# Optimization experiments

Hardware: AMD Instinct MI355X
Metric: run time of the kernel (lower is better)

Reference implementation:

```python
import jax, jax.numpy as jnp
import numpy as np

H = 256
W = 256
P = 512

# spherical-harmonics constants (degree 0..3), as in the 3DGS CUDA kernel
C0 = 0.28209479177387814
C1 = 0.4886025119029199
C2 = [1.0925484305920792, -1.0925484305920792, 0.31539156525252005, -1.0925484305920792, 0.5462742152960396]
C3 = [-0.5900435899266435, 2.890611442640554, -0.4570457994644658, 0.3731763325901154, -0.4570457994644658, 1.445305721320277, -0.5900435899266435]


def _quat_to_rot(q):
    # q: [P,4] (w,x,y,z), normalized here as the kernel assumes unit quats
    q = q / jnp.linalg.norm(q, axis=-1, keepdims=True)
    w, x, y, z = q[:, 0], q[:, 1], q[:, 2], q[:, 3]
    R = jnp.stack([
        1 - 2 * (y * y + z * z), 2 * (x * y - w * z), 2 * (x * z + w * y),
        2 * (x * y + w * z), 1 - 2 * (x * x + z * z), 2 * (y * z - w * x),
        2 * (x * z - w * y), 2 * (y * z + w * x), 1 - 2 * (x * x + y * y)], axis=-1)
    return R.reshape(-1, 3, 3)


def _eval_sh(sh, d):
    # sh: [P,16,3], d: [P,3] unit view dirs -> RGB [P,3]
    x, y, z = d[:, 0:1], d[:, 1:2], d[:, 2:3]
    xx, yy, zz = x * x, y * y, z * z
    xy, yz, xz = x * y, y * z, x * z
    res = C0 * sh[:, 0]
    res = res - C1 * y * sh[:, 1] + C1 * z * sh[:, 2] - C1 * x * sh[:, 3]
    res = (res + C2[0] * xy * sh[:, 4] + C2[1] * yz * sh[:, 5]
           + C2[2] * (2 * zz - xx - yy) * sh[:, 6] + C2[3] * xz * sh[:, 7]
           + C2[4] * (xx - yy) * sh[:, 8])
    res = (res + C3[0] * y * (3 * xx - yy) * sh[:, 9] + C3[1] * xy * z * sh[:, 10]
           + C3[2] * y * (4 * zz - xx - yy) * sh[:, 11]
           + C3[3] * z * (2 * zz - 3 * xx - 3 * yy) * sh[:, 12]
           + C3[4] * x * (4 * zz - xx - yy) * sh[:, 13]
           + C3[5] * z * (xx - yy) * sh[:, 14] + C3[6] * x * (xx - 3 * yy) * sh[:, 15])
    return jnp.maximum(res + 0.5, 0.0)


def render(means_3d, features, opacities, scales, rotations, viewmatrix, projmatrix, campos, tanfovx, tanfovy):
    Rv = viewmatrix[:3, :3]
    tv = viewmatrix[:3, 3]
    t = means_3d @ Rv.T + tv            # camera-space positions [P,3]
    depth = t[:, 2]
    # 3D covariance = (R S)(R S)^T
    Rq = _quat_to_rot(rotations)
    M = Rq * scales[:, None, :]
    cov3 = M @ jnp.swapaxes(M, 1, 2)    # [P,3,3]
    # EWA 2D covariance via perspective Jacobian
    fx = W / (2.0 * tanfovx)
    fy = H / (2.0 * tanfovy)
    limx = 1.3 * tanfovx
    limy = 1.3 * tanfovy
    tz = depth
    txz = jnp.clip(t[:, 0] / tz, -limx, limx) * tz
    tyz = jnp.clip(t[:, 1] / tz, -limy, limy) * tz
    zeros = jnp.zeros_like(tz)
    J = jnp.stack([
        jnp.stack([fx / tz, zeros, -fx * txz / (tz * tz)], -1),
        jnp.stack([zeros, fy / tz, -fy * tyz / (tz * tz)], -1)], 1)  # [P,2,3]
    T = J @ Rv
    cov2 = T @ cov3 @ jnp.swapaxes(T, 1, 2)  # [P,2,2]
    a = cov2[:, 0, 0] + 0.3  # low-pass dilation as in 3DGS
    b = cov2[:, 0, 1]
    c = cov2[:, 1, 1] + 0.3
    det = a * c - b * b
    inv_det = 1.0 / jnp.where(det > 0, det, 1.0)
    conic_a = c * inv_det
    conic_b = -b * inv_det
    conic_c = a * inv_det
    # project means to pixel coords
    ph = jnp.concatenate([means_3d, jnp.ones_like(depth)[:, None]], 1)
    pp = ph @ projmatrix.T
    pw = pp[:, 3] + 1e-7
    px = ((pp[:, 0] / pw + 1.0) * W - 1.0) * 0.5
    py = ((pp[:, 1] / pw + 1.0) * H - 1.0) * 0.5
    # SH -> RGB with view direction
    dirs = means_3d - campos
    dirs = dirs / jnp.linalg.norm(dirs, axis=-1, keepdims=True)
    colors = _eval_sh(features, dirs)   # [P,3]
    valid = (depth > 0.2) & (det > 0)
    # global front-to-back depth sort (kernel does per-tile; one global tile here)
    order = jnp.argsort(depth)
    px, py = px[order], py[order]
    conic_a, conic_b, conic_c = conic_a[order], conic_b[order], conic_c[order]
    colors = colors[order]
    opa = opacities[:, 0][order]
    valid = valid[order]
    # per-pixel alpha compositing
    ys, xs = jnp.meshgrid(jnp.arange(H, dtype=px.dtype), jnp.arange(W, dtype=px.dtype), indexing='ij')
    pix_x = xs.reshape(-1)              # [HW]
    pix_y = ys.reshape(-1)
    dx = pix_x[:, None] - px[None, :]   # [HW,P]
    dy = pix_y[:, None] - py[None, :]
    power = -0.5 * (conic_a[None, :] * dx * dx + conic_c[None, :] * dy * dy) - conic_b[None, :] * dx * dy
    alpha = jnp.minimum(0.99, opa[None, :] * jnp.exp(power))
    alpha = jnp.where((power <= 0.0) & valid[None, :] & (alpha >= 1.0 / 255.0), alpha, 0.0)
    Tcum = jnp.cumprod(1.0 - alpha, axis=1)                 # transmittance after gaussian i
    T_excl = jnp.concatenate([jnp.ones((alpha.shape[0], 1), alpha.dtype), Tcum[:, :-1]], 1)
    wgt = alpha * T_excl                                    # [HW,P]
    bg = jnp.ones((3,), dtype=alpha.dtype)                  # bg_color = (1,1,1) as in module
    out = wgt @ colors + Tcum[:, -1:] * bg[None, :]         # [HW,3]
    return out.T.reshape(3, H, W)


def setup_inputs() -> dict:
    key = jax.random.key(0)
    k = jax.random.split(key, 5)
    means_3d = jax.random.normal(k[0], (P, 3), jnp.float32) * jnp.array([1.5, 1.5, 0.8]) + jnp.array([0.0, 0.0, 5.0])
    features = jax.random.normal(k[1], (P, 16, 3), jnp.float32) * 0.3
    opacities = jax.random.uniform(k[2], (P, 1), jnp.float32) * 0.9 + 0.05
    scales = jax.random.uniform(k[3], (P, 3), jnp.float32) * 0.08 + 0.02
    rotations = jax.random.normal(k[4], (P, 4), jnp.float32)
    fov = np.radians(60.0)
    tanfov = np.float32(np.tan(fov * 0.5))
    near, far = 0.1, 100.0
    proj = np.array([[1.0 / tanfov, 0, 0, 0],
                     [0, 1.0 / tanfov, 0, 0],
                     [0, 0, far / (far - near), -(far * near) / (far - near)],
                     [0, 0, 1.0, 0]], np.float32)
    viewmatrix = jnp.eye(4, dtype=jnp.float32)  # camera at origin looking +z
    projmatrix = jnp.asarray(proj)              # world->clip (view is identity)
    campos = jnp.zeros((3,), jnp.float32)
    return {"means_3d": means_3d, "features": features, "opacities": opacities,
            "scales": scales, "rotations": rotations, "viewmatrix": viewmatrix,
            "projmatrix": projmatrix, "campos": campos,
            "tanfovx": jnp.float32(tanfov), "tanfovy": jnp.float32(tanfov)}


def reference(means_3d, features, opacities, scales, rotations, viewmatrix, projmatrix, campos, tanfovx, tanfovy):
    return render(means_3d, features, opacities, scales, rotations, viewmatrix, projmatrix, campos, tanfovx, tanfovy)
```

## Files before the change

kernel.cpp:

```cpp
#include <hip/hip_runtime.h>
#include <hip/hip_bf16.h>

#define PQ 512
#define HH 256
#define WW 256

__global__ __launch_bounds__(256) void gs_fused_kernel(
    const float* __restrict__ means, const float* __restrict__ feats,
    const float* __restrict__ opac, const float* __restrict__ scales,
    const float* __restrict__ rots, const float* __restrict__ vm,
    const float* __restrict__ pm, const float* __restrict__ campos,
    const float* __restrict__ tfx, const float* __restrict__ tfy,
    float* __restrict__ out)
{
    __shared__ unsigned long long cKey[PQ];
    __shared__ int   cGi[PQ];
    __shared__ float cPx[PQ], cNa[PQ], cU[PQ], cV[PQ], cOp[PQ];
    __shared__ float4 SA[PQ], SB[PQ];
    __shared__ int s_cnt[4], s_base[5];

    const int tid  = threadIdx.x;
    const int wid  = tid >> 6;
    const int lane = tid & 63;
    const float fy = (float)blockIdx.x;

    const float tanfovx = *tfx, tanfovy = *tfy;
    const float fxs = WW / (2.0f*tanfovx), fys = HH / (2.0f*tanfovy);
    const float limx = 1.3f*tanfovx, limy = 1.3f*tanfovy;

    float rPx[2], rNa[2], rU[2], rV[2], rOp[2];
    unsigned long long rKey[2], m[2];
    bool kp[2];
    int cnt = 0;

    #pragma unroll
    for (int r = 0; r < 2; ++r) {
        const int g = r*256 + tid;
        const float mx = means[3*g], my = means[3*g+1], mz = means[3*g+2];

        const float tx = vm[0]*mx + vm[1]*my + vm[2]*mz + vm[3];
        const float ty = vm[4]*mx + vm[5]*my + vm[6]*mz + vm[7];
        const float tz = vm[8]*mx + vm[9]*my + vm[10]*mz + vm[11];
        const float depth = tz;

        const float4 q = *reinterpret_cast<const float4*>(rots + 4*g);
        float qw = q.x, qx = q.y, qy = q.z, qz = q.w;
        const float qn = 1.0f / sqrtf(qw*qw + qx*qx + qy*qy + qz*qz);
        qw *= qn; qx *= qn; qy *= qn; qz *= qn;
        const float R00 = 1.0f - 2.0f*(qy*qy + qz*qz), R01 = 2.0f*(qx*qy - qw*qz), R02 = 2.0f*(qx*qz + qw*qy);
        const float R10 = 2.0f*(qx*qy + qw*qz), R11 = 1.0f - 2.0f*(qx*qx + qz*qz), R12 = 2.0f*(qy*qz - qw*qx);
        const float R20 = 2.0f*(qx*qz - qw*qy), R21 = 2.0f*(qy*qz + qw*qx), R22 = 1.0f - 2.0f*(qx*qx + qy*qy);

        const float s0 = scales[3*g], s1 = scales[3*g+1], s2 = scales[3*g+2];
        const float Sx = s0*s0, Sy = s1*s1, Sz = s2*s2;
        const float c00 = R00*R00*Sx + R01*R01*Sy + R02*R02*Sz;
        const float c01 = R00*R10*Sx + R01*R11*Sy + R02*R12*Sz;
        const float c02 = R00*R20*Sx + R01*R21*Sy + R02*R22*Sz;
        const float c11 = R10*R10*Sx + R11*R11*Sy + R12*R12*Sz;
        const float c12 = R10*R20*Sx + R11*R21*Sy + R12*R22*Sz;
        const float c22 = R20*R20*Sx + R21*R21*Sy + R22*R22*Sz;

        const float invz = 1.0f / tz;
        const float txz = fminf(fmaxf(tx*invz, -limx), limx) * tz;
        const float tyz = fminf(fmaxf(ty*invz, -limy), limy) * tz;
        const float J00 = fxs*invz, J02 = -fxs*txz*invz*invz;
        const float J11 = fys*invz, J12 = -fys*tyz*invz*invz;
        const float T00 = J00*vm[0] + J02*vm[8];
        const float T01 = J00*vm[1] + J02*vm[9];
        const float T02 = J00*vm[2] + J02*vm[10];
        const float T10 = J11*vm[4] + J12*vm[8];
        const float T11 = J11*vm[5] + J12*vm[9];
        const float T12 = J11*vm[6] + J12*vm[10];
        const float u0 = c00*T00 + c01*T01 + c02*T02;
        const float u1 = c01*T00 + c11*T01 + c12*T02;
        const float u2 = c02*T00 + c12*T01 + c22*T02;
        const float v0 = c00*T10 + c01*T11 + c02*T12;
        const float v1 = c01*T10 + c11*T11 + c12*T12;
        const float v2 = c02*T10 + c12*T11 + c22*T12;
        const float a  = T00*u0 + T01*u1 + T02*u2 + 0.3f;
        const float b  = T10*u0 + T11*u1 + T12*u2;
        const float c  = T10*v0 + T11*v1 + T12*v2 + 0.3f;
        const float det = a*c - b*b;
        const bool valid = (depth > 0.2f) && (det > 0.0f);
        const float inv_det = 1.0f / (det > 0.0f ? det : 1.0f);
        const float ca = c*inv_det, cbq = -b*inv_det, cc = a*inv_det;

        const float pw = pm[12]*mx + pm[13]*my + pm[14]*mz + pm[15] + 1e-7f;
        const float p0 = pm[0]*mx + pm[1]*my + pm[2]*mz + pm[3];
        const float p1 = pm[4]*mx + pm[5]*my + pm[6]*mz + pm[7];
        const float px = ((p0/pw + 1.0f)*WW - 1.0f)*0.5f;
        const float py = ((p1/pw + 1.0f)*HH - 1.0f)*0.5f;

        const float opa_ = valid ? opac[g] : 0.0f;

        const float lmin = 0.25f*(ca + cc) - sqrtf(0.0625f*(ca - cc)*(ca - cc) + 0.25f*cbq*cbq);
        const float thr = __logf(255.0f * opa_);
        float rmax2;
        if (valid && thr > 0.0f)
            rmax2 = (lmin > 0.0f) ? (thr/lmin)*1.02f + 1e-4f : 3.4e38f;
        else
            rmax2 = 0.0f;

        const float dy  = fy - py;
        const float dxn = fmaxf(0.0f, fmaxf(-px, px - (float)(WW-1)));
        kp[r] = (fmaf(dy, dy, dxn*dxn) <= rmax2);

        rPx[r] = px;
        rNa[r] = -0.5f*ca;
        rU[r]  = -cbq*dy;
        rV[r]  = (-0.5f*cc)*dy*dy;
        rOp[r] = opa_;

        const unsigned int fb = __float_as_uint(depth);
        const unsigned int ks = fb ^ ((fb >> 31) ? 0xFFFFFFFFu : 0x80000000u);
        rKey[r] = ((unsigned long long)ks << 32) | (unsigned int)g;

        m[r] = __ballot(kp[r]);
        cnt += __popcll(m[r]);
    }

    if (lane == 0) s_cnt[wid] = cnt;
    __syncthreads();
    if (tid == 0) {
        int s = 0;
        #pragma unroll
        for (int w = 0; w < 4; ++w) { s_base[w] = s; s += s_cnt[w]; }
        s_base[4] = s;
    }
    __syncthreads();

    int pos = s_base[wid];
    #pragma unroll
    for (int r = 0; r < 2; ++r) {
        if (kp[r]) {
            const int p = pos + __popcll(m[r] & ((1ULL << lane) - 1ULL));
            cKey[p] = rKey[r]; cGi[p] = r*256 + tid;
            cPx[p] = rPx[r]; cNa[p] = rNa[r]; cU[p] = rU[r]; cV[p] = rV[r]; cOp[p] = rOp[r];
        }
        pos += __popcll(m[r]);
    }
    __syncthreads();

    const int n = s_base[4];

    for (int j = tid; j < n; j += 256) {
        const unsigned long long kj = cKey[j];
        int rk = 0;
        for (int i = 0; i < n; ++i) rk += (cKey[i] < kj) ? 1 : 0;

        const int g = cGi[j];
        const float mx = means[3*g], my = means[3*g+1], mz = means[3*g+2];
        const float ddx = mx - campos[0], ddy = my - campos[1], ddz = mz - campos[2];
        const float dn = 1.0f / sqrtf(ddx*ddx + ddy*ddy + ddz*ddz);
        const float x = ddx*dn, y = ddy*dn, z = ddz*dn;
        const float xx = x*x, yy = y*y, zz = z*z, xy = x*y, yz = y*z, xz = x*z;
        float bas[16];
        bas[0]  = 0.28209479177387814f;
        bas[1]  = -0.4886025119029199f*y;
        bas[2]  = 0.4886025119029199f*z;
        bas[3]  = -0.4886025119029199f*x;
        bas[4]  = 1.0925484305920792f*xy;
        bas[5]  = -1.0925484305920792f*yz;
        bas[6]  = 0.31539156525252005f*(2.0f*zz - xx - yy);
        bas[7]  = -1.0925484305920792f*xz;
        bas[8]  = 0.5462742152960396f*(xx - yy);
        bas[9]  = -0.5900435899266435f*y*(3.0f*xx - yy);
        bas[10] = 2.890611442640554f*xy*z;
        bas[11] = -0.4570457994644658f*y*(4.0f*zz - xx - yy);
        bas[12] = 0.3731763325901154f*z*(2.0f*zz - 3.0f*xx - 3.0f*yy);
        bas[13] = -0.4570457994644658f*x*(4.0f*zz - xx - yy);
        bas[14] = 1.445305721320277f*z*(xx - yy);
        bas[15] = -0.5900435899266435f*x*(xx - 3.0f*yy);

        float fv[48];
        const float4* fp = reinterpret_cast<const float4*>(feats + 48*g);
        #pragma unroll
        for (int qq = 0; qq < 12; ++qq)
            *reinterpret_cast<float4*>(&fv[4*qq]) = fp[qq];

        float colr = 0.0f, colg = 0.0f, colb = 0.0f;
        #pragma unroll
        for (int k = 0; k < 16; ++k) {
            colr += bas[k]*fv[k*3+0];
            colg += bas[k]*fv[k*3+1];
            colb += bas[k]*fv[k*3+2];
        }
        colr = fmaxf(colr + 0.5f, 0.0f);
        colg = fmaxf(colg + 0.5f, 0.0f);
        colb = fmaxf(colb + 0.5f, 0.0f);

        SA[rk] = make_float4(cPx[j], cNa[j], cU[j], cV[j]);
        SB[rk] = make_float4(cOp[j], colr, colg, colb);
    }
    __syncthreads();

    const float fx = (float)tid;
    float T = 1.0f, accr = 0.0f, accg = 0.0f, accb = 0.0f;
    #pragma unroll 4
    for (int j = 0; j < n; ++j) {
        const float4 A = SA[j];
        const float4 B = SB[j];
        const float dx  = fx - A.x;
        const float pwr = fmaf(fmaf(A.y, dx, A.z), dx, A.w);
        const float gg  = __expf(pwr);
        const float al  = fminf(0.99f, B.x*gg);
        const bool  ok  = (pwr <= 0.0f) && (al >= (1.0f/255.0f));
        const float w   = ok ? al*T : 0.0f;
        accr = fmaf(w, B.y, accr);
        accg = fmaf(w, B.z, accg);
        accb = fmaf(w, B.w, accb);
        T -= w;
    }

    const int pix = blockIdx.x*WW + tid;
    out[pix]            = accr + T;
    out[HH*WW + pix]    = accg + T;
    out[2*HH*WW + pix]  = accb + T;
}

extern "C" void kernel_launch(void* const* d_in, const int* in_sizes, int n_in,
                              void* d_out, int out_size, void* d_ws, size_t ws_size,
                              hipStream_t stream) {
    const float* means  = (const float*)d_in[0];
    const float* feats  = (const float*)d_in[1];
    const float* opac   = (const float*)d_in[2];
    const float* scales = (const float*)d_in[3];
    const float* rots   = (const float*)d_in[4];
    const float* vm     = (const float*)d_in[5];
    const float* pm     = (const float*)d_in[6];
    const float* campos = (const float*)d_in[7];
    const float* tfx    = (const float*)d_in[8];
    const float* tfy    = (const float*)d_in[9];

    gs_fused_kernel<<<HH, 256, 0, stream>>>(means, feats, opac, scales, rots, vm, pm,
                                            campos, tfx, tfy, (float*)d_out);
}
```

Before: 13.51 us.

## Split per-pixel compositing across four depth segments with 1024-thread blocks

Blocks grow from 256 to 1024 threads. Each gaussian's preprocessing gets its own thread, and each surviving gaussian's rank/SH evaluation also runs once per thread. The front-to-back blend for each pixel is split into four contiguous depth segments. Each segment accumulates color and transmittance, and the partial results are merged through shared memory in order. The aim is to shorten the serial per-pixel loop and per-thread preprocessing, at the cost of an extra sync, more shared memory, and larger blocks that may limit occupancy and register budget. Early termination is not present, so every segment does full work.

New measurement: 12.01 us. -11.1%, faster.

```diff
diff --git a/kernel.cpp b/kernel.cpp
--- a/kernel.cpp
+++ b/kernel.cpp
@@ -5,7 +5,7 @@
 #define HH 256
 #define WW 256
 
-__global__ __launch_bounds__(256) void gs_fused_kernel(
+__global__ __launch_bounds__(1024) void gs_fused_kernel(
     const float* __restrict__ means, const float* __restrict__ feats,
     const float* __restrict__ opac, const float* __restrict__ scales,
     const float* __restrict__ rots, const float* __restrict__ vm,
@@ -17,7 +17,8 @@
     __shared__ int   cGi[PQ];
     __shared__ float cPx[PQ], cNa[PQ], cU[PQ], cV[PQ], cOp[PQ];
     __shared__ float4 SA[PQ], SB[PQ];
-    __shared__ int s_cnt[4], s_base[5];
+    __shared__ float4 comb[4][WW];
+    __shared__ int s_cnt[8], s_base[9];
 
     const int tid  = threadIdx.x;
     const int wid  = tid >> 6;
@@ -28,14 +29,12 @@
     const float fxs = WW / (2.0f*tanfovx), fys = HH / (2.0f*tanfovy);
     const float limx = 1.3f*tanfovx, limy = 1.3f*tanfovy;
 
-    float rPx[2], rNa[2], rU[2], rV[2], rOp[2];
-    unsigned long long rKey[2], m[2];
-    bool kp[2];
-    int cnt = 0;
-
-    #pragma unroll
-    for (int r = 0; r < 2; ++r) {
-        const int g = r*256 + tid;
+    float rPx = 0.f, rNa = 0.f, rU = 0.f, rV = 0.f, rOp = 0.f;
+    unsigned long long rKey = 0, m = 0;
+    bool kp = false;
+
+    if (tid < PQ) {
+        const int g = tid;
         const float mx = means[3*g], my = means[3*g+1], mz = means[3*g+2];
 
         const float tx = vm[0]*mx + vm[1]*my + vm[2]*mz + vm[3];
@@ -103,47 +102,41 @@
 
         const float dy  = fy - py;
         const float dxn = fmaxf(0.0f, fmaxf(-px, px - (float)(WW-1)));
-        kp[r] = (fmaf(dy, dy, dxn*dxn) <= rmax2);
-
-        rPx[r] = px;
-        rNa[r] = -0.5f*ca;
-        rU[r]  = -cbq*dy;
-        rV[r]  = (-0.5f*cc)*dy*dy;
-        rOp[r] = opa_;
+        kp = (fmaf(dy, dy, dxn*dxn) <= rmax2);
+
+        rPx = px;
+        rNa = -0.5f*ca;
+        rU  = -cbq*dy;
+        rV  = (-0.5f*cc)*dy*dy;
+        rOp = opa_;
 
         const unsigned int fb = __float_as_uint(depth);
         const unsigned int ks = fb ^ ((fb >> 31) ? 0xFFFFFFFFu : 0x80000000u);
-        rKey[r] = ((unsigned long long)ks << 32) | (unsigned int)g;
-
-        m[r] = __ballot(kp[r]);
-        cnt += __popcll(m[r]);
-    }
-
-    if (lane == 0) s_cnt[wid] = cnt;
+        rKey = ((unsigned long long)ks << 32) | (unsigned int)g;
+
+        m = __ballot(kp);
+        if (lane == 0) s_cnt[wid] = __popcll(m);
+    }
     __syncthreads();
     if (tid == 0) {
         int s = 0;
         #pragma unroll
-        for (int w = 0; w < 4; ++w) { s_base[w] = s; s += s_cnt[w]; }
-        s_base[4] = s;
-    }
-    __syncthreads();
-
-    int pos = s_base[wid];
-    #pragma unroll
-    for (int r = 0; r < 2; ++r) {
-        if (kp[r]) {
-            const int p = pos + __popcll(m[r] & ((1ULL << lane) - 1ULL));
-            cKey[p] = rKey[r]; cGi[p] = r*256 + tid;
-            cPx[p] = rPx[r]; cNa[p] = rNa[r]; cU[p] = rU[r]; cV[p] = rV[r]; cOp[p] = rOp[r];
-        }
-        pos += __popcll(m[r]);
-    }
-    __syncthreads();
-
-    const int n = s_base[4];
-
-    for (int j = tid; j < n; j += 256) {
+        for (int w = 0; w < 8; ++w) { s_base[w] = s; s += s_cnt[w]; }
+        s_base[8] = s;
+    }
+    __syncthreads();
+
+    if (tid < PQ && kp) {
+        const int p = s_base[wid] + __popcll(m & ((1ULL << lane) - 1ULL));
+        cKey[p] = rKey; cGi[p] = tid;
+        cPx[p] = rPx; cNa[p] = rNa; cU[p] = rU; cV[p] = rV; cOp[p] = rOp;
+    }
+    __syncthreads();
+
+    const int n = s_base[8];
+
+    if (tid < n) {
+        const int j = tid;
         const unsigned long long kj = cKey[j];
         int rk = 0;
         for (int i = 0; i < n; ++i) rk += (cKey[i] < kj) ? 1 : 0;
@@ -194,10 +187,15 @@
     }
     __syncthreads();
 
-    const float fx = (float)tid;
+    const int q   = tid >> 8;
+    const int pix = tid & 255;
+    const float fx = (float)pix;
+    const int nq = (n + 3) >> 2;
+    const int j0 = q*nq;
+    const int j1 = min(n, j0 + nq);
+
     float T = 1.0f, accr = 0.0f, accg = 0.0f, accb = 0.0f;
-    #pragma unroll 4
-    for (int j = 0; j < n; ++j) {
+    for (int j = j0; j < j1; ++j) {
         const float4 A = SA[j];
         const float4 B = SB[j];
         const float dx  = fx - A.x;
@@ -211,11 +209,24 @@
         accb = fmaf(w, B.w, accb);
         T -= w;
     }
-
-    const int pix = blockIdx.x*WW + tid;
-    out[pix]            = accr + T;
-    out[HH*WW + pix]    = accg + T;
-    out[2*HH*WW + pix]  = accb + T;
+    comb[q][pix] = make_float4(accr, accg, accb, T);
+    __syncthreads();
+
+    if (tid < WW) {
+        float Tt = 1.0f, r = 0.0f, g = 0.0f, b = 0.0f;
+        #pragma unroll
+        for (int s = 0; s < 4; ++s) {
+            const float4 c = comb[s][tid];
+            r = fmaf(Tt, c.x, r);
+            g = fmaf(Tt, c.y, g);
+            b = fmaf(Tt, c.z, b);
+            Tt *= c.w;
+        }
+        const int p = blockIdx.x*WW + tid;
+        out[p]            = r + Tt;
+        out[HH*WW + p]    = g + Tt;
+        out[2*HH*WW + p]  = b + Tt;
+    }
 }
 
 extern "C" void kernel_launch(void* const* d_in, const int* in_sizes, int n_in,
@@ -232,6 +243,6 @@
     const float* tfx    = (const float*)d_in[8];
     const float* tfy    = (const float*)d_in[9];
 
-    gs_fused_kernel<<<HH, 256, 0, stream>>>(means, feats, opac, scales, rots, vm, pm,
-                                            campos, tfx, tfy, (float*)d_out);
+    gs_fused_kernel<<<HH, 1024, 0, stream>>>(means, feats, opac, scales, rots, vm, pm,
+                                             campos, tfx, tfy, (float*)d_out);
 }
```
